# Kernel optimization log

Measured on AMD Instinct MI355X. Metric: run time of the kernel, lower is better.

The kernel has to match this reference:

```python
import jax, jax.numpy as jnp
import numpy as np

E, H, F, T, K = 32, 1024, 512, 1024, 8

def setup_inputs() -> dict:
    key = jax.random.key(0)
    k1, k2, k3, k4, k5 = jax.random.split(key, 5)
    return {
        "hidden_states": jax.random.normal(k1, (T, H), dtype=jnp.float32),
        "top_k_index": jax.random.randint(k2, (T, K), 0, E),
        "top_k_weights": jax.random.uniform(k3, (T, K), dtype=jnp.float32),
        "gate_up_proj": jax.random.normal(k4, (E, 2 * F, H), dtype=jnp.float32),
        "down_proj": jax.random.normal(k5, (E, H, F), dtype=jnp.float32),
    }

def reference(hidden_states, top_k_index, top_k_weights, gate_up_proj, down_proj):
    n_experts = gate_up_proj.shape[0]
    T_ = hidden_states.shape[0]
    # Combine routing weights into dense [T, E] map (duplicates accumulate,
    # matching torch's index_add_ semantics).
    w = jnp.zeros((T_, n_experts), dtype=hidden_states.dtype)
    w = w.at[jnp.arange(T_)[:, None], top_k_index].add(top_k_weights)
    ffn = down_proj.shape[-1]

    def step(final, params):
        Wgu, Wd, we = params  # [2F,H], [H,F], [T]
        gu = hidden_states @ Wgu.T            # [T, 2F]
        gate, up = gu[:, :ffn], gu[:, ffn:]
        out = (jax.nn.silu(gate) * up) @ Wd.T  # [T, H]
        return final + we[:, None] * out, None

    final, _ = jax.lax.scan(step, jnp.zeros_like(hidden_states),
                            (gate_up_proj, down_proj, w.T))
    return final
```

## Files before the change

kernel.cpp:

```cpp
#include <hip/hip_runtime.h>
#include <hip/hip_bf16.h>

#define NE     32
#define HD     1024
#define FF     512
#define NT     1024
#define TOPK   8
#define NPAIR  (NT * TOPK)
#define MAXT2  96

typedef __attribute__((ext_vector_type(8))) short  bf16x8;
typedef __attribute__((ext_vector_type(4))) float  f32x4;

__device__ __forceinline__ unsigned short f2bf_rne(float f) {
    unsigned u = __float_as_uint(f);
    u += 0x7FFFu + ((u >> 16) & 1u);
    return (unsigned short)(u >> 16);
}

__device__ __forceinline__ unsigned pk2(float x, float y) {
    __hip_bfloat162 h = __float22bfloat162_rn(float2{x, y});
    union { __hip_bfloat162 h; unsigned u; } c;
    c.h = h;
    return c.u;
}

__device__ __forceinline__ uint4 pk8(const float* __restrict__ p) {
    float4 a = *(const float4*)p;
    float4 b = *(const float4*)(p + 4);
    uint4 r;
    r.x = pk2(a.x, a.y);
    r.y = pk2(a.z, a.w);
    r.z = pk2(b.x, b.y);
    r.w = pk2(b.z, b.w);
    return r;
}


__global__ __launch_bounds__(1024) void k_route(const int* __restrict__ idx,
                                                const float* __restrict__ tkw,
                                                int* __restrict__ meta) {
    __shared__ int sc[NE], scur[NE], soff[NE + 1];
    __shared__ int ste[MAXT2], stm[MAXT2], snt;
    int tid = threadIdx.x;
    if (tid < NE) { sc[tid] = 0; scur[tid] = 0; }
    __syncthreads();
    int e8[TOPK];
#pragma unroll
    for (int j = 0; j < TOPK; j++) { e8[j] = idx[tid * TOPK + j]; atomicAdd(&sc[e8[j]], 1); }
    __syncthreads();
    if (tid == 0) {
        int off = 0, nt = 0;
        for (int e = 0; e < NE; e++) {
            soff[e] = off;
            for (int s = 0; s < sc[e]; s += 128) { ste[nt] = e; stm[nt] = s; nt++; }
            off += sc[e];
        }
        soff[NE] = off; snt = nt;
    }
    __syncthreads();
    int*   tok_list = meta + 256;
    float* w_list   = (float*)(meta + 8448);
    int*   posmap   = meta + 16640;
#pragma unroll
    for (int j = 0; j < TOPK; j++) {
        int e = e8[j];
        int p = soff[e] + atomicAdd(&scur[e], 1);
        tok_list[p] = tid;
        w_list[p]   = tkw[tid * TOPK + j];
        posmap[tid * TOPK + j] = p;
    }
    if (tid <= NE) meta[1 + tid] = soff[tid];
    if (tid == 0)  meta[0] = snt;
    if (tid < MAXT2) { meta[64 + tid] = (tid < snt) ? ste[tid] : 0;
                       meta[160 + tid] = (tid < snt) ? stm[tid] : 0; }
}

__global__ __launch_bounds__(256) void k_mm1(
        const float* __restrict__ hs, const float* __restrict__ wgu,
        const int* __restrict__ meta, unsigned short* __restrict__ A) {
    int numt = meta[0];
    int bx = blockIdx.x;
    if (bx >= numt) return;
    int e   = meta[64 + bx], m0 = meta[160 + bx];
    int seg = meta[1 + e];
    int nrows = meta[1 + e + 1] - seg - m0;
    if (nrows > 128) nrows = 128;
    int c0 = blockIdx.y * 64;
    const int* tok_list = meta + 256;
    const float* w_list = (const float*)(meta + 8448);

    __shared__ __align__(16) unsigned short Xs[128][40];
    __shared__ __align__(16) unsigned short Ws[128][40];
    __shared__ int   toks[128];
    __shared__ float wrow[128];
    int tid = threadIdx.x;
    if (tid < 128) {
        toks[tid] = (tid < nrows) ? tok_list[seg + m0 + tid] : -1;
        wrow[tid] = (tid < nrows) ? w_list[seg + m0 + tid] : 0.f;
    }
    __syncthreads();

    int wave = tid >> 6, lane = tid & 63, lr = lane & 15, lk = lane >> 4;
    f32x4 accg[2][4] = {}, accu[2][4] = {};
    const float* wbase = wgu + (size_t)e * 2 * FF * HD;

    for (int k0 = 0; k0 < HD; k0 += 32) {
        for (int c = tid; c < 512; c += 256) {
            int r = c >> 2, cc = c & 3;
            int tk = toks[r];
            uint4 xv = make_uint4(0, 0, 0, 0);
            if (tk >= 0) xv = pk8(hs + (size_t)tk * HD + k0 + cc * 8);
            *(uint4*)&Xs[r][cc * 8] = xv;
            int grow = (r < 64) ? (c0 + r) : (FF + c0 + (r - 64));
            *(uint4*)&Ws[r][cc * 8] = pk8(wbase + (size_t)grow * HD + k0 + cc * 8);
        }
        __syncthreads();
        bf16x8 a0 = *(const bf16x8*)&Xs[wave * 32 + lr][lk * 8];
        bf16x8 a1 = *(const bf16x8*)&Xs[wave * 32 + 16 + lr][lk * 8];
#pragma unroll
        for (int cf = 0; cf < 4; cf++) {
            bf16x8 bg = *(const bf16x8*)&Ws[cf * 16 + lr][lk * 8];
            bf16x8 bu = *(const bf16x8*)&Ws[64 + cf * 16 + lr][lk * 8];
            accg[0][cf] = __builtin_amdgcn_mfma_f32_16x16x32_bf16(a0, bg, accg[0][cf], 0, 0, 0);
            accg[1][cf] = __builtin_amdgcn_mfma_f32_16x16x32_bf16(a1, bg, accg[1][cf], 0, 0, 0);
            accu[0][cf] = __builtin_amdgcn_mfma_f32_16x16x32_bf16(a0, bu, accu[0][cf], 0, 0, 0);
            accu[1][cf] = __builtin_amdgcn_mfma_f32_16x16x32_bf16(a1, bu, accu[1][cf], 0, 0, 0);
        }
        __syncthreads();
    }
#pragma unroll
    for (int rf = 0; rf < 2; rf++)
#pragma unroll
        for (int q = 0; q < 4; q++) {
            int r = wave * 32 + rf * 16 + lk * 4 + q;
            if (r < nrows) {
                float w = wrow[r];
#pragma unroll
                for (int cf = 0; cf < 4; cf++) {
                    float g = accg[rf][cf][q], u = accu[rf][cf][q];
                    float act = (g / (1.f + __expf(-g))) * u * w;
                    A[(size_t)(seg + m0 + r) * FF + c0 + cf * 16 + lr] = f2bf_rne(act);
                }
            }
        }
}

__global__ __launch_bounds__(256) void k_mm2(
        const unsigned short* __restrict__ A, const float* __restrict__ wd,
        const int* __restrict__ meta, float* __restrict__ O) {
    int numt = meta[0];
    int bx = blockIdx.x;
    if (bx >= numt) return;
    int e   = meta[64 + bx], m0 = meta[160 + bx];
    int seg = meta[1 + e];
    int nrows = meta[1 + e + 1] - seg - m0;
    if (nrows > 128) nrows = 128;
    int n0 = blockIdx.y * 128;

    __shared__ __align__(16) unsigned short Xs[128][40];
    __shared__ __align__(16) unsigned short Ws[128][40];
    int tid = threadIdx.x;
    int wave = tid >> 6, lane = tid & 63, lr = lane & 15, lk = lane >> 4;
    f32x4 acc[2][8] = {};
    const float* wbase = wd + (size_t)e * HD * FF;

    for (int k0 = 0; k0 < FF; k0 += 32) {
        for (int c = tid; c < 512; c += 256) {
            int r = c >> 2, cc = c & 3;
            uint4 xv = make_uint4(0, 0, 0, 0);
            if (r < nrows) xv = *(const uint4*)(A + (size_t)(seg + m0 + r) * FF + k0 + cc * 8);
            *(uint4*)&Xs[r][cc * 8] = xv;
            *(uint4*)&Ws[r][cc * 8] = pk8(wbase + (size_t)(n0 + r) * FF + k0 + cc * 8);
        }
        __syncthreads();
        bf16x8 a0 = *(const bf16x8*)&Xs[wave * 32 + lr][lk * 8];
        bf16x8 a1 = *(const bf16x8*)&Xs[wave * 32 + 16 + lr][lk * 8];
#pragma unroll
        for (int cf = 0; cf < 8; cf++) {
            bf16x8 b = *(const bf16x8*)&Ws[cf * 16 + lr][lk * 8];
            acc[0][cf] = __builtin_amdgcn_mfma_f32_16x16x32_bf16(a0, b, acc[0][cf], 0, 0, 0);
            acc[1][cf] = __builtin_amdgcn_mfma_f32_16x16x32_bf16(a1, b, acc[1][cf], 0, 0, 0);
        }
        __syncthreads();
    }
#pragma unroll
    for (int rf = 0; rf < 2; rf++)
#pragma unroll
        for (int q = 0; q < 4; q++) {
            int r = wave * 32 + rf * 16 + lk * 4 + q;
            if (r < nrows) {
#pragma unroll
                for (int cf = 0; cf < 8; cf++)
                    O[(size_t)(seg + m0 + r) * HD + n0 + cf * 16 + lr] = acc[rf][cf][q];
            }
        }
}

__global__ void k_reduce(const float* __restrict__ O, const int* __restrict__ posmap,
                         float* __restrict__ out) {
    int i = blockIdx.x * blockDim.x + threadIdx.x;
    int t = i >> 8, c4 = i & 255;
    float4 acc = make_float4(0.f, 0.f, 0.f, 0.f);
#pragma unroll
    for (int k = 0; k < TOPK; k++) {
        int p = posmap[t * TOPK + k];
        float4 v = ((const float4*)(O + (size_t)p * HD))[c4];
        acc.x += v.x; acc.y += v.y; acc.z += v.z; acc.w += v.w;
    }
    ((float4*)out)[i] = acc;
}

extern "C" void kernel_launch(void* const* d_in, const int* in_sizes, int n_in,
                              void* d_out, int out_size, void* d_ws, size_t ws_size,
                              hipStream_t stream) {
    const float* hs  = (const float*)d_in[0];
    const int*   idx = (const int*)  d_in[1];
    const float* tkw = (const float*)d_in[2];
    const float* wgu = (const float*)d_in[3];
    const float* wd  = (const float*)d_in[4];
    float* out = (float*)d_out;

    const size_t OFF_A = 128 * 1024;
    const size_t OFF_O = OFF_A + (size_t)NPAIR * FF * 2;

    char* ws = (char*)d_ws;
    int* meta = (int*)ws;
    unsigned short* A_bf = (unsigned short*)(ws + OFF_A);
    float* O_rows        = (float*)(ws + OFF_O);
    const int* posmap    = meta + 16640;

    k_route<<<1, 1024, 0, stream>>>(idx, tkw, meta);
    dim3 g1(MAXT2, FF / 64);
    k_mm1<<<g1, 256, 0, stream>>>(hs, wgu, meta, A_bf);
    dim3 g2(MAXT2, HD / 128);
    k_mm2<<<g2, 256, 0, stream>>>(A_bf, wd, meta, O_rows);
    k_reduce<<<NT * HD / 4 / 256, 256, 0, stream>>>(O_rows, posmap, out);
}
```

Measured before the change: 133.6 us.

## Double-buffer LDS tiles, halve N-tile width, and swizzle block order in grouped GEMMs

Both grouped GEMM kernels now prefetch the next K-slice from global memory into registers while MFMAs run on the current LDS buffer. Each iteration writes into a second LDS buffer, so one barrier per iteration is removed. The output-column tile is halved, doubling the grid, and block indices are remapped so that neighbouring blocks share experts and rows for L2 reuse. The trade-off is that each weight tile's X rows are loaded twice as often, and each block does less MFMA work per iteration.

New measurement: 393.3 us. +194.4%, slower.

```diff
diff --git a/kernel.cpp b/kernel.cpp
--- a/kernel.cpp
+++ b/kernel.cpp
@@ -17,24 +17,19 @@
     u += 0x7FFFu + ((u >> 16) & 1u);
     return (unsigned short)(u >> 16);
 }
-
 __device__ __forceinline__ unsigned pk2(float x, float y) {
     __hip_bfloat162 h = __float22bfloat162_rn(float2{x, y});
     union { __hip_bfloat162 h; unsigned u; } c;
     c.h = h;
     return c.u;
 }
-
-__device__ __forceinline__ uint4 pk8(const float* __restrict__ p) {
-    float4 a = *(const float4*)p;
-    float4 b = *(const float4*)(p + 4);
+__device__ __forceinline__ uint4 pk8v(float4 a, float4 b) {
     uint4 r;
-    r.x = pk2(a.x, a.y);
-    r.y = pk2(a.z, a.w);
-    r.z = pk2(b.x, b.y);
-    r.w = pk2(b.z, b.w);
+    r.x = pk2(a.x, a.y); r.y = pk2(a.z, a.w);
+    r.z = pk2(b.x, b.y); r.w = pk2(b.z, b.w);
     return r;
 }
+#define MFMA16(a, b, c) __builtin_amdgcn_mfma_f32_16x16x32_bf16(a, b, c, 0, 0, 0)
 
 
 __global__ __launch_bounds__(1024) void k_route(const int* __restrict__ idx,
@@ -79,55 +74,86 @@
 __global__ __launch_bounds__(256) void k_mm1(
         const float* __restrict__ hs, const float* __restrict__ wgu,
         const int* __restrict__ meta, unsigned short* __restrict__ A) {
+    int lid = blockIdx.y * MAXT2 + blockIdx.x;
+    int wsw = (lid & 7) * 192 + (lid >> 3);
+    int bx = wsw % MAXT2, by = wsw / MAXT2;
     int numt = meta[0];
-    int bx = blockIdx.x;
     if (bx >= numt) return;
     int e   = meta[64 + bx], m0 = meta[160 + bx];
     int seg = meta[1 + e];
-    int nrows = meta[1 + e + 1] - seg - m0;
+    int nrows = meta[2 + e] - seg - m0;
     if (nrows > 128) nrows = 128;
-    int c0 = blockIdx.y * 64;
+    int c0 = by * 32;
+
+    __shared__ __align__(16) unsigned short Xs[2][128][40];
+    __shared__ __align__(16) unsigned short Ws[2][64][40];
+    __shared__ int   toks[128];
+    __shared__ float wrows[128];
+    int tid = threadIdx.x;
     const int* tok_list = meta + 256;
     const float* w_list = (const float*)(meta + 8448);
-
-    __shared__ __align__(16) unsigned short Xs[128][40];
-    __shared__ __align__(16) unsigned short Ws[128][40];
-    __shared__ int   toks[128];
-    __shared__ float wrow[128];
-    int tid = threadIdx.x;
     if (tid < 128) {
-        toks[tid] = (tid < nrows) ? tok_list[seg + m0 + tid] : -1;
-        wrow[tid] = (tid < nrows) ? w_list[seg + m0 + tid] : 0.f;
-    }
-    __syncthreads();
+        toks[tid]  = (tid < nrows) ? tok_list[seg + m0 + tid] : -1;
+        wrows[tid] = (tid < nrows) ? w_list[seg + m0 + tid] : 0.f;
+    }
+    __syncthreads();
+
+    int xr1 = tid >> 2, xc = (tid & 3) * 8;
+    int xr2 = xr1 + 64;
+    int tk1 = toks[xr1], tk2 = toks[xr2];
+    const float* xp1 = hs + (size_t)tk1 * HD + xc;
+    const float* xp2 = hs + (size_t)tk2 * HD + xc;
+    int wr = tid >> 2;
+    int wg_row = (wr < 32) ? (c0 + wr) : (FF + c0 + (wr - 32));
+    const float* wp = wgu + (size_t)e * (2 * FF) * HD + (size_t)wg_row * HD + xc;
 
     int wave = tid >> 6, lane = tid & 63, lr = lane & 15, lk = lane >> 4;
-    f32x4 accg[2][4] = {}, accu[2][4] = {};
-    const float* wbase = wgu + (size_t)e * 2 * FF * HD;
-
+    f32x4 accg[2][2] = {}, accu[2][2] = {};
+    const float4 z4 = {0.f, 0.f, 0.f, 0.f};
+
+    {
+        float4 a1 = tk1 >= 0 ? *(const float4*)(xp1)     : z4;
+        float4 b1 = tk1 >= 0 ? *(const float4*)(xp1 + 4) : z4;
+        float4 a2 = tk2 >= 0 ? *(const float4*)(xp2)     : z4;
+        float4 b2 = tk2 >= 0 ? *(const float4*)(xp2 + 4) : z4;
+        float4 wa = *(const float4*)(wp), wb = *(const float4*)(wp + 4);
+        *(uint4*)&Xs[0][xr1][xc] = pk8v(a1, b1);
+        *(uint4*)&Xs[0][xr2][xc] = pk8v(a2, b2);
+        *(uint4*)&Ws[0][wr][xc]  = pk8v(wa, wb);
+    }
+    __syncthreads();
+
+    int cur = 0;
     for (int k0 = 0; k0 < HD; k0 += 32) {
-        for (int c = tid; c < 512; c += 256) {
-            int r = c >> 2, cc = c & 3;
-            int tk = toks[r];
-            uint4 xv = make_uint4(0, 0, 0, 0);
-            if (tk >= 0) xv = pk8(hs + (size_t)tk * HD + k0 + cc * 8);
-            *(uint4*)&Xs[r][cc * 8] = xv;
-            int grow = (r < 64) ? (c0 + r) : (FF + c0 + (r - 64));
-            *(uint4*)&Ws[r][cc * 8] = pk8(wbase + (size_t)grow * HD + k0 + cc * 8);
+        bool more = (k0 + 32) < HD;
+        float4 a1, b1, a2, b2, wa, wb;
+        if (more) {
+            int k = k0 + 32;
+            a1 = tk1 >= 0 ? *(const float4*)(xp1 + k)     : z4;
+            b1 = tk1 >= 0 ? *(const float4*)(xp1 + k + 4) : z4;
+            a2 = tk2 >= 0 ? *(const float4*)(xp2 + k)     : z4;
+            b2 = tk2 >= 0 ? *(const float4*)(xp2 + k + 4) : z4;
+            wa = *(const float4*)(wp + k);
+            wb = *(const float4*)(wp + k + 4);
+        }
+        bf16x8 fa0 = *(const bf16x8*)&Xs[cur][wave * 32 + lr][lk * 8];
+        bf16x8 fa1 = *(const bf16x8*)&Xs[cur][wave * 32 + 16 + lr][lk * 8];
+#pragma unroll
+        for (int cf = 0; cf < 2; cf++) {
+            bf16x8 bg = *(const bf16x8*)&Ws[cur][cf * 16 + lr][lk * 8];
+            bf16x8 bu = *(const bf16x8*)&Ws[cur][32 + cf * 16 + lr][lk * 8];
+            accg[0][cf] = MFMA16(fa0, bg, accg[0][cf]);
+            accg[1][cf] = MFMA16(fa1, bg, accg[1][cf]);
+            accu[0][cf] = MFMA16(fa0, bu, accu[0][cf]);
+            accu[1][cf] = MFMA16(fa1, bu, accu[1][cf]);
+        }
+        if (more) {
+            *(uint4*)&Xs[cur ^ 1][xr1][xc] = pk8v(a1, b1);
+            *(uint4*)&Xs[cur ^ 1][xr2][xc] = pk8v(a2, b2);
+            *(uint4*)&Ws[cur ^ 1][wr][xc]  = pk8v(wa, wb);
         }
         __syncthreads();
-        bf16x8 a0 = *(const bf16x8*)&Xs[wave * 32 + lr][lk * 8];
-        bf16x8 a1 = *(const bf16x8*)&Xs[wave * 32 + 16 + lr][lk * 8];
-#pragma unroll
-        for (int cf = 0; cf < 4; cf++) {
-            bf16x8 bg = *(const bf16x8*)&Ws[cf * 16 + lr][lk * 8];
-            bf16x8 bu = *(const bf16x8*)&Ws[64 + cf * 16 + lr][lk * 8];
-            accg[0][cf] = __builtin_amdgcn_mfma_f32_16x16x32_bf16(a0, bg, accg[0][cf], 0, 0, 0);
-            accg[1][cf] = __builtin_amdgcn_mfma_f32_16x16x32_bf16(a1, bg, accg[1][cf], 0, 0, 0);
-            accu[0][cf] = __builtin_amdgcn_mfma_f32_16x16x32_bf16(a0, bu, accu[0][cf], 0, 0, 0);
-            accu[1][cf] = __builtin_amdgcn_mfma_f32_16x16x32_bf16(a1, bu, accu[1][cf], 0, 0, 0);
-        }
-        __syncthreads();
+        cur ^= 1;
     }
 #pragma unroll
     for (int rf = 0; rf < 2; rf++)
@@ -135,9 +161,9 @@
         for (int q = 0; q < 4; q++) {
             int r = wave * 32 + rf * 16 + lk * 4 + q;
             if (r < nrows) {
-                float w = wrow[r];
-#pragma unroll
-                for (int cf = 0; cf < 4; cf++) {
+                float w = wrows[r];
+#pragma unroll
+                for (int cf = 0; cf < 2; cf++) {
                     float g = accg[rf][cf][q], u = accu[rf][cf][q];
                     float act = (g / (1.f + __expf(-g))) * u * w;
                     A[(size_t)(seg + m0 + r) * FF + c0 + cf * 16 + lr] = f2bf_rne(act);
@@ -149,40 +175,68 @@
 __global__ __launch_bounds__(256) void k_mm2(
         const unsigned short* __restrict__ A, const float* __restrict__ wd,
         const int* __restrict__ meta, float* __restrict__ O) {
+    int lid = blockIdx.y * MAXT2 + blockIdx.x;
+    int wsw = (lid & 7) * 192 + (lid >> 3);
+    int bx = wsw % MAXT2, by = wsw / MAXT2;
     int numt = meta[0];
-    int bx = blockIdx.x;
     if (bx >= numt) return;
     int e   = meta[64 + bx], m0 = meta[160 + bx];
     int seg = meta[1 + e];
-    int nrows = meta[1 + e + 1] - seg - m0;
+    int nrows = meta[2 + e] - seg - m0;
     if (nrows > 128) nrows = 128;
-    int n0 = blockIdx.y * 128;
-
-    __shared__ __align__(16) unsigned short Xs[128][40];
-    __shared__ __align__(16) unsigned short Ws[128][40];
+    int n0 = by * 64;
+
+    __shared__ __align__(16) unsigned short Xs[2][128][40];
+    __shared__ __align__(16) unsigned short Ws[2][64][40];
     int tid = threadIdx.x;
+    int xr1 = tid >> 2, xc = (tid & 3) * 8;
+    int xr2 = xr1 + 64;
+    bool v1 = xr1 < nrows, v2 = xr2 < nrows;
+    const unsigned short* ap1 = A + (size_t)(seg + m0 + xr1) * FF + xc;
+    const unsigned short* ap2 = A + (size_t)(seg + m0 + xr2) * FF + xc;
+    int wr = tid >> 2;
+    const float* wp = wd + (size_t)e * HD * FF + (size_t)(n0 + wr) * FF + xc;
+
     int wave = tid >> 6, lane = tid & 63, lr = lane & 15, lk = lane >> 4;
-    f32x4 acc[2][8] = {};
-    const float* wbase = wd + (size_t)e * HD * FF;
-
+    f32x4 acc[2][4] = {};
+    const uint4  zu = {0u, 0u, 0u, 0u};
+
+    {
+        uint4 x1 = v1 ? *(const uint4*)(ap1) : zu;
+        uint4 x2 = v2 ? *(const uint4*)(ap2) : zu;
+        float4 wa = *(const float4*)(wp), wb = *(const float4*)(wp + 4);
+        *(uint4*)&Xs[0][xr1][xc] = x1;
+        *(uint4*)&Xs[0][xr2][xc] = x2;
+        *(uint4*)&Ws[0][wr][xc]  = pk8v(wa, wb);
+    }
+    __syncthreads();
+
+    int cur = 0;
     for (int k0 = 0; k0 < FF; k0 += 32) {
-        for (int c = tid; c < 512; c += 256) {
-            int r = c >> 2, cc = c & 3;
-            uint4 xv = make_uint4(0, 0, 0, 0);
-            if (r < nrows) xv = *(const uint4*)(A + (size_t)(seg + m0 + r) * FF + k0 + cc * 8);
-            *(uint4*)&Xs[r][cc * 8] = xv;
-            *(uint4*)&Ws[r][cc * 8] = pk8(wbase + (size_t)(n0 + r) * FF + k0 + cc * 8);
+        bool more = (k0 + 32) < FF;
+        uint4 x1, x2; float4 wa, wb;
+        if (more) {
+            int k = k0 + 32;
+            x1 = v1 ? *(const uint4*)(ap1 + k) : zu;
+            x2 = v2 ? *(const uint4*)(ap2 + k) : zu;
+            wa = *(const float4*)(wp + k);
+            wb = *(const float4*)(wp + k + 4);
+        }
+        bf16x8 fa0 = *(const bf16x8*)&Xs[cur][wave * 32 + lr][lk * 8];
+        bf16x8 fa1 = *(const bf16x8*)&Xs[cur][wave * 32 + 16 + lr][lk * 8];
+#pragma unroll
+        for (int cf = 0; cf < 4; cf++) {
+            bf16x8 b = *(const bf16x8*)&Ws[cur][cf * 16 + lr][lk * 8];
+            acc[0][cf] = MFMA16(fa0, b, acc[0][cf]);
+            acc[1][cf] = MFMA16(fa1, b, acc[1][cf]);
+        }
+        if (more) {
+            *(uint4*)&Xs[cur ^ 1][xr1][xc] = x1;
+            *(uint4*)&Xs[cur ^ 1][xr2][xc] = x2;
+            *(uint4*)&Ws[cur ^ 1][wr][xc]  = pk8v(wa, wb);
         }
         __syncthreads();
-        bf16x8 a0 = *(const bf16x8*)&Xs[wave * 32 + lr][lk * 8];
-        bf16x8 a1 = *(const bf16x8*)&Xs[wave * 32 + 16 + lr][lk * 8];
-#pragma unroll
-        for (int cf = 0; cf < 8; cf++) {
-            bf16x8 b = *(const bf16x8*)&Ws[cf * 16 + lr][lk * 8];
-            acc[0][cf] = __builtin_amdgcn_mfma_f32_16x16x32_bf16(a0, b, acc[0][cf], 0, 0, 0);
-            acc[1][cf] = __builtin_amdgcn_mfma_f32_16x16x32_bf16(a1, b, acc[1][cf], 0, 0, 0);
-        }
-        __syncthreads();
+        cur ^= 1;
     }
 #pragma unroll
     for (int rf = 0; rf < 2; rf++)
@@ -191,7 +245,7 @@
             int r = wave * 32 + rf * 16 + lk * 4 + q;
             if (r < nrows) {
 #pragma unroll
-                for (int cf = 0; cf < 8; cf++)
+                for (int cf = 0; cf < 4; cf++)
                     O[(size_t)(seg + m0 + r) * HD + n0 + cf * 16 + lr] = acc[rf][cf][q];
             }
         }
@@ -231,9 +285,9 @@
     const int* posmap    = meta + 16640;
 
     k_route<<<1, 1024, 0, stream>>>(idx, tkw, meta);
-    dim3 g1(MAXT2, FF / 64);
+    dim3 g1(MAXT2, FF / 32);
     k_mm1<<<g1, 256, 0, stream>>>(hs, wgu, meta, A_bf);
-    dim3 g2(MAXT2, HD / 128);
+    dim3 g2(MAXT2, HD / 64);
     k_mm2<<<g2, 256, 0, stream>>>(A_bf, wd, meta, O_rows);
     k_reduce<<<NT * HD / 4 / 256, 256, 0, stream>>>(O_rows, posmap, out);
 }
```

## Pre-gather bf16 tokens and pipeline MoE GEMMs with direct-to-LDS triple buffering

Applied to the files above, without the earlier changes.

Adds a gather kernel that converts routed token rows to bf16 once. Both grouped GEMMs now stream activations with global_load_lds into a triple-buffered, XOR-swizzled LDS ring, and keep weights in registers with a double-buffered prefetch, so there is one barrier per k-step instead of two. Block indices are remapped so blocks sharing an expert run close together, and the kernels use launch bounds for two blocks per CU. The aim is to hide global latency and stop converting the same fp32 activations repeatedly per column tile. In exchange it adds a kernel launch and an extra bf16 workspace, and relies on hand-written vmcnt waits being correct.

Result: slower. 140.6 us (+5.3%).

```diff
diff --git a/kernel.cpp b/kernel.cpp
--- a/kernel.cpp
+++ b/kernel.cpp
@@ -17,25 +17,40 @@
     u += 0x7FFFu + ((u >> 16) & 1u);
     return (unsigned short)(u >> 16);
 }
-
 __device__ __forceinline__ unsigned pk2(float x, float y) {
     __hip_bfloat162 h = __float22bfloat162_rn(float2{x, y});
     union { __hip_bfloat162 h; unsigned u; } c;
     c.h = h;
     return c.u;
 }
-
-__device__ __forceinline__ uint4 pk8(const float* __restrict__ p) {
-    float4 a = *(const float4*)p;
-    float4 b = *(const float4*)(p + 4);
+__device__ __forceinline__ uint4 pk8q(float4 a, float4 b) {
     uint4 r;
-    r.x = pk2(a.x, a.y);
-    r.y = pk2(a.z, a.w);
-    r.z = pk2(b.x, b.y);
-    r.w = pk2(b.z, b.w);
+    r.x = pk2(a.x, a.y); r.y = pk2(a.z, a.w);
+    r.z = pk2(b.x, b.y); r.w = pk2(b.z, b.w);
     return r;
 }
-
+__device__ __forceinline__ bf16x8 pk8r(float4 a, float4 b) {
+    union { unsigned u[4]; bf16x8 v; } r;
+    r.u[0] = pk2(a.x, a.y); r.u[1] = pk2(a.z, a.w);
+    r.u[2] = pk2(b.x, b.y); r.u[3] = pk2(b.z, b.w);
+    return r.v;
+}
+__device__ __forceinline__ void gload16(const void* g, void* l) {
+    __builtin_amdgcn_global_load_lds(
+        (const __attribute__((address_space(1))) unsigned int*)g,
+        (__attribute__((address_space(3))) unsigned int*)l, 16, 0, 0);
+}
+#define MFMA16(a, b, c) __builtin_amdgcn_mfma_f32_16x16x32_bf16(a, b, c, 0, 0, 0)
+
+#define PIPE_SYNC() do {                                   \
+    asm volatile("s_waitcnt vmcnt(6)" ::: "memory");       \
+    __builtin_amdgcn_s_barrier();                          \
+    __builtin_amdgcn_sched_barrier(0);                     \
+} while (0)
+
+#define OFF_XG (128u * 1024u)
+#define OFF_AB (OFF_XG + 8320u * 2048u)
+#define OFF_O  (OFF_AB + 8320u * 1024u)
 
 __global__ __launch_bounds__(1024) void k_route(const int* __restrict__ idx,
                                                 const float* __restrict__ tkw,
@@ -76,123 +91,210 @@
                        meta[160 + tid] = (tid < snt) ? stm[tid] : 0; }
 }
 
-__global__ __launch_bounds__(256) void k_mm1(
-        const float* __restrict__ hs, const float* __restrict__ wgu,
-        const int* __restrict__ meta, unsigned short* __restrict__ A) {
+__global__ void k_gather(const float* __restrict__ hs, const int* __restrict__ meta,
+                         unsigned short* __restrict__ Xg) {
+    int i = blockIdx.x * blockDim.x + threadIdx.x;
+    int p = i >> 7, c = (i & 127) << 3;
+    int tok = meta[256 + p];
+    float4 a = *(const float4*)(hs + (size_t)tok * HD + c);
+    float4 b = *(const float4*)(hs + (size_t)tok * HD + c + 4);
+    *(uint4*)(Xg + (size_t)p * HD + c) = pk8q(a, b);
+}
+
+__global__ __launch_bounds__(256, 2) void k_mm1(
+        const unsigned short* __restrict__ Xg, const float* __restrict__ wgu,
+        const int* __restrict__ meta, const float* __restrict__ w_list,
+        unsigned short* __restrict__ A) {
+    int lid = blockIdx.x;
+    int wsw = (lid & 7) * 96 + (lid >> 3);
+    int bx = wsw >> 3, by = wsw & 7;
     int numt = meta[0];
-    int bx = blockIdx.x;
     if (bx >= numt) return;
     int e   = meta[64 + bx], m0 = meta[160 + bx];
     int seg = meta[1 + e];
-    int nrows = meta[1 + e + 1] - seg - m0;
+    int nrows = meta[2 + e] - seg - m0;
     if (nrows > 128) nrows = 128;
-    int c0 = blockIdx.y * 64;
-    const int* tok_list = meta + 256;
-    const float* w_list = (const float*)(meta + 8448);
-
-    __shared__ __align__(16) unsigned short Xs[128][40];
-    __shared__ __align__(16) unsigned short Ws[128][40];
-    __shared__ int   toks[128];
-    __shared__ float wrow[128];
+    int c0 = by * 64;
+
+    __shared__ __align__(16) unsigned char Xb0[8192];
+    __shared__ __align__(16) unsigned char Xb1[8192];
+    __shared__ __align__(16) unsigned char Xb2[8192];
     int tid = threadIdx.x;
-    if (tid < 128) {
-        toks[tid] = (tid < nrows) ? tok_list[seg + m0 + tid] : -1;
-        wrow[tid] = (tid < nrows) ? w_list[seg + m0 + tid] : 0.f;
-    }
-    __syncthreads();
-
     int wave = tid >> 6, lane = tid & 63, lr = lane & 15, lk = lane >> 4;
-    f32x4 accg[2][4] = {}, accu[2][4] = {};
-    const float* wbase = wgu + (size_t)e * 2 * FF * HD;
-
-    for (int k0 = 0; k0 < HD; k0 += 32) {
-        for (int c = tid; c < 512; c += 256) {
-            int r = c >> 2, cc = c & 3;
-            int tk = toks[r];
-            uint4 xv = make_uint4(0, 0, 0, 0);
-            if (tk >= 0) xv = pk8(hs + (size_t)tk * HD + k0 + cc * 8);
-            *(uint4*)&Xs[r][cc * 8] = xv;
-            int grow = (r < 64) ? (c0 + r) : (FF + c0 + (r - 64));
-            *(uint4*)&Ws[r][cc * 8] = pk8(wbase + (size_t)grow * HD + k0 + cc * 8);
-        }
-        __syncthreads();
-        bf16x8 a0 = *(const bf16x8*)&Xs[wave * 32 + lr][lk * 8];
-        bf16x8 a1 = *(const bf16x8*)&Xs[wave * 32 + 16 + lr][lk * 8];
-#pragma unroll
-        for (int cf = 0; cf < 4; cf++) {
-            bf16x8 bg = *(const bf16x8*)&Ws[cf * 16 + lr][lk * 8];
-            bf16x8 bu = *(const bf16x8*)&Ws[64 + cf * 16 + lr][lk * 8];
-            accg[0][cf] = __builtin_amdgcn_mfma_f32_16x16x32_bf16(a0, bg, accg[0][cf], 0, 0, 0);
-            accg[1][cf] = __builtin_amdgcn_mfma_f32_16x16x32_bf16(a1, bg, accg[1][cf], 0, 0, 0);
-            accu[0][cf] = __builtin_amdgcn_mfma_f32_16x16x32_bf16(a0, bu, accu[0][cf], 0, 0, 0);
-            accu[1][cf] = __builtin_amdgcn_mfma_f32_16x16x32_bf16(a1, bu, accu[1][cf], 0, 0, 0);
-        }
-        __syncthreads();
-    }
-#pragma unroll
-    for (int rf = 0; rf < 2; rf++)
+
+    unsigned Lp0 = (unsigned)(wave * 2) * 1024u + (unsigned)lane * 16u;
+    unsigned Lp1 = Lp0 + 1024u;
+    unsigned ldsoff0 = Lp0, ldsoff1 = Lp1;
+    const unsigned char* xsrc0 = (const unsigned char*)Xg +
+        (size_t)(seg + m0 + (Lp0 >> 6)) * (HD * 2) + ((Lp0 & 63u) ^ (((Lp0 >> 7) & 3u) << 4));
+    const unsigned char* xsrc1 = (const unsigned char*)Xg +
+        (size_t)(seg + m0 + (Lp1 >> 6)) * (HD * 2) + ((Lp1 & 63u) ^ (((Lp1 >> 7) & 3u) << 4));
+
+    int cp = c0 + wave * 16 + lr;
+    const float* gp = wgu + ((size_t)e * 2 * FF + cp) * HD + lk * 8;
+    const float* up = gp + (size_t)FF * HD;
+
+    unsigned aoff[8];
+#pragma unroll
+    for (int mf = 0; mf < 8; mf++) {
+        unsigned row = mf * 16 + lr;
+        aoff[mf] = row * 64 + (((unsigned)lk * 16) ^ (((row >> 1) & 3u) << 4));
+    }
+
+    f32x4 acc[8][2] = {};
+    float4 wsA[4], wsB[4];
+    const unsigned char* cur = Xb0;
+    const unsigned char* nxt = Xb1;
+    const unsigned char* fut = Xb2;
+
+    gload16(xsrc0, Xb0 + ldsoff0); gload16(xsrc1, Xb0 + ldsoff1);
+    xsrc0 += 64; xsrc1 += 64;
+    gload16(xsrc0, Xb1 + ldsoff0); gload16(xsrc1, Xb1 + ldsoff1);
+    xsrc0 += 64; xsrc1 += 64;
+    wsA[0] = *(const float4*)(gp);     wsA[1] = *(const float4*)(gp + 4);
+    wsA[2] = *(const float4*)(up);     wsA[3] = *(const float4*)(up + 4);
+    int wk = 32;
+
+    auto step = [&](float4 (&wuse)[4], float4 (&wld)[4], bool doX, bool doW) {
+        PIPE_SYNC();
+        if (doX) {
+            gload16(xsrc0, (void*)(fut + ldsoff0));
+            gload16(xsrc1, (void*)(fut + ldsoff1));
+            xsrc0 += 64; xsrc1 += 64;
+        }
+        if (doW) {
+            wld[0] = *(const float4*)(gp + wk);     wld[1] = *(const float4*)(gp + wk + 4);
+            wld[2] = *(const float4*)(up + wk);     wld[3] = *(const float4*)(up + wk + 4);
+            wk += 32;
+        }
+        bf16x8 bg = pk8r(wuse[0], wuse[1]);
+        bf16x8 bu = pk8r(wuse[2], wuse[3]);
+#pragma unroll
+        for (int mf = 0; mf < 8; mf++) {
+            bf16x8 af = *(const bf16x8*)(cur + aoff[mf]);
+            acc[mf][0] = MFMA16(af, bg, acc[mf][0]);
+            acc[mf][1] = MFMA16(af, bu, acc[mf][1]);
+        }
+        const unsigned char* t = cur; cur = nxt; nxt = fut; fut = t;
+    };
+
+    for (int t2 = 0; t2 < 14; t2++) {
+        step(wsA, wsB, true, true);
+        step(wsB, wsA, true, true);
+    }
+    step(wsA, wsB, true,  true);
+    step(wsB, wsA, true,  true);
+    step(wsA, wsB, false, true);
+    step(wsB, wsA, false, false);
+
+#pragma unroll
+    for (int mf = 0; mf < 8; mf++)
 #pragma unroll
         for (int q = 0; q < 4; q++) {
-            int r = wave * 32 + rf * 16 + lk * 4 + q;
+            int r = mf * 16 + lk * 4 + q;
             if (r < nrows) {
-                float w = wrow[r];
-#pragma unroll
-                for (int cf = 0; cf < 4; cf++) {
-                    float g = accg[rf][cf][q], u = accu[rf][cf][q];
-                    float act = (g / (1.f + __expf(-g))) * u * w;
-                    A[(size_t)(seg + m0 + r) * FF + c0 + cf * 16 + lr] = f2bf_rne(act);
-                }
+                float w = w_list[seg + m0 + r];
+                float g = acc[mf][0][q], u = acc[mf][1][q];
+                float act = (g / (1.f + __expf(-g))) * u * w;
+                A[(size_t)(seg + m0 + r) * FF + cp] = f2bf_rne(act);
             }
         }
 }
 
-__global__ __launch_bounds__(256) void k_mm2(
+__global__ __launch_bounds__(256, 2) void k_mm2(
         const unsigned short* __restrict__ A, const float* __restrict__ wd,
         const int* __restrict__ meta, float* __restrict__ O) {
+    int lid = blockIdx.x;
+    int wsw = (lid & 7) * 96 + (lid >> 3);
+    int bx = wsw >> 3, by = wsw & 7;
     int numt = meta[0];
-    int bx = blockIdx.x;
     if (bx >= numt) return;
     int e   = meta[64 + bx], m0 = meta[160 + bx];
     int seg = meta[1 + e];
-    int nrows = meta[1 + e + 1] - seg - m0;
+    int nrows = meta[2 + e] - seg - m0;
     if (nrows > 128) nrows = 128;
-    int n0 = blockIdx.y * 128;
-
-    __shared__ __align__(16) unsigned short Xs[128][40];
-    __shared__ __align__(16) unsigned short Ws[128][40];
+    int n0 = by * 128;
+
+    __shared__ __align__(16) unsigned char Xb0[8192];
+    __shared__ __align__(16) unsigned char Xb1[8192];
+    __shared__ __align__(16) unsigned char Xb2[8192];
     int tid = threadIdx.x;
     int wave = tid >> 6, lane = tid & 63, lr = lane & 15, lk = lane >> 4;
-    f32x4 acc[2][8] = {};
-    const float* wbase = wd + (size_t)e * HD * FF;
-
-    for (int k0 = 0; k0 < FF; k0 += 32) {
-        for (int c = tid; c < 512; c += 256) {
-            int r = c >> 2, cc = c & 3;
-            uint4 xv = make_uint4(0, 0, 0, 0);
-            if (r < nrows) xv = *(const uint4*)(A + (size_t)(seg + m0 + r) * FF + k0 + cc * 8);
-            *(uint4*)&Xs[r][cc * 8] = xv;
-            *(uint4*)&Ws[r][cc * 8] = pk8(wbase + (size_t)(n0 + r) * FF + k0 + cc * 8);
-        }
-        __syncthreads();
-        bf16x8 a0 = *(const bf16x8*)&Xs[wave * 32 + lr][lk * 8];
-        bf16x8 a1 = *(const bf16x8*)&Xs[wave * 32 + 16 + lr][lk * 8];
-#pragma unroll
-        for (int cf = 0; cf < 8; cf++) {
-            bf16x8 b = *(const bf16x8*)&Ws[cf * 16 + lr][lk * 8];
-            acc[0][cf] = __builtin_amdgcn_mfma_f32_16x16x32_bf16(a0, b, acc[0][cf], 0, 0, 0);
-            acc[1][cf] = __builtin_amdgcn_mfma_f32_16x16x32_bf16(a1, b, acc[1][cf], 0, 0, 0);
-        }
-        __syncthreads();
-    }
-#pragma unroll
-    for (int rf = 0; rf < 2; rf++)
+
+    unsigned Lp0 = (unsigned)(wave * 2) * 1024u + (unsigned)lane * 16u;
+    unsigned Lp1 = Lp0 + 1024u;
+    unsigned ldsoff0 = Lp0, ldsoff1 = Lp1;
+    const unsigned char* xsrc0 = (const unsigned char*)A +
+        (size_t)(seg + m0 + (Lp0 >> 6)) * (FF * 2) + ((Lp0 & 63u) ^ (((Lp0 >> 7) & 3u) << 4));
+    const unsigned char* xsrc1 = (const unsigned char*)A +
+        (size_t)(seg + m0 + (Lp1 >> 6)) * (FF * 2) + ((Lp1 & 63u) ^ (((Lp1 >> 7) & 3u) << 4));
+
+    int n_a = n0 + wave * 32 + lr;
+    int n_b = n_a + 16;
+    const float* wpa = wd + ((size_t)e * HD + n_a) * FF + lk * 8;
+    const float* wpb = wd + ((size_t)e * HD + n_b) * FF + lk * 8;
+
+    unsigned aoff[8];
+#pragma unroll
+    for (int mf = 0; mf < 8; mf++) {
+        unsigned row = mf * 16 + lr;
+        aoff[mf] = row * 64 + (((unsigned)lk * 16) ^ (((row >> 1) & 3u) << 4));
+    }
+
+    f32x4 acc[8][2] = {};
+    float4 wsA[4], wsB[4];
+    const unsigned char* cur = Xb0;
+    const unsigned char* nxt = Xb1;
+    const unsigned char* fut = Xb2;
+
+    gload16(xsrc0, Xb0 + ldsoff0); gload16(xsrc1, Xb0 + ldsoff1);
+    xsrc0 += 64; xsrc1 += 64;
+    gload16(xsrc0, Xb1 + ldsoff0); gload16(xsrc1, Xb1 + ldsoff1);
+    xsrc0 += 64; xsrc1 += 64;
+    wsA[0] = *(const float4*)(wpa);    wsA[1] = *(const float4*)(wpa + 4);
+    wsA[2] = *(const float4*)(wpb);    wsA[3] = *(const float4*)(wpb + 4);
+    int wk = 32;
+
+    auto step = [&](float4 (&wuse)[4], float4 (&wld)[4], bool doX, bool doW) {
+        PIPE_SYNC();
+        if (doX) {
+            gload16(xsrc0, (void*)(fut + ldsoff0));
+            gload16(xsrc1, (void*)(fut + ldsoff1));
+            xsrc0 += 64; xsrc1 += 64;
+        }
+        if (doW) {
+            wld[0] = *(const float4*)(wpa + wk);   wld[1] = *(const float4*)(wpa + wk + 4);
+            wld[2] = *(const float4*)(wpb + wk);   wld[3] = *(const float4*)(wpb + wk + 4);
+            wk += 32;
+        }
+        bf16x8 b0 = pk8r(wuse[0], wuse[1]);
+        bf16x8 b1 = pk8r(wuse[2], wuse[3]);
+#pragma unroll
+        for (int mf = 0; mf < 8; mf++) {
+            bf16x8 af = *(const bf16x8*)(cur + aoff[mf]);
+            acc[mf][0] = MFMA16(af, b0, acc[mf][0]);
+            acc[mf][1] = MFMA16(af, b1, acc[mf][1]);
+        }
+        const unsigned char* t = cur; cur = nxt; nxt = fut; fut = t;
+    };
+
+    for (int t2 = 0; t2 < 6; t2++) {
+        step(wsA, wsB, true, true);
+        step(wsB, wsA, true, true);
+    }
+    step(wsA, wsB, true,  true);
+    step(wsB, wsA, true,  true);
+    step(wsA, wsB, false, true);
+    step(wsB, wsA, false, false);
+
+#pragma unroll
+    for (int mf = 0; mf < 8; mf++)
 #pragma unroll
         for (int q = 0; q < 4; q++) {
-            int r = wave * 32 + rf * 16 + lk * 4 + q;
+            int r = mf * 16 + lk * 4 + q;
             if (r < nrows) {
-#pragma unroll
-                for (int cf = 0; cf < 8; cf++)
-                    O[(size_t)(seg + m0 + r) * HD + n0 + cf * 16 + lr] = acc[rf][cf][q];
+                O[(size_t)(seg + m0 + r) * HD + n_a] = acc[mf][0][q];
+                O[(size_t)(seg + m0 + r) * HD + n_b] = acc[mf][1][q];
             }
         }
 }
@@ -221,19 +323,17 @@
     const float* wd  = (const float*)d_in[4];
     float* out = (float*)d_out;
 
-    const size_t OFF_A = 128 * 1024;
-    const size_t OFF_O = OFF_A + (size_t)NPAIR * FF * 2;
-
     char* ws = (char*)d_ws;
     int* meta = (int*)ws;
-    unsigned short* A_bf = (unsigned short*)(ws + OFF_A);
+    unsigned short* Xg   = (unsigned short*)(ws + OFF_XG);
+    unsigned short* A_bf = (unsigned short*)(ws + OFF_AB);
     float* O_rows        = (float*)(ws + OFF_O);
+    const float* w_list  = (const float*)(meta + 8448);
     const int* posmap    = meta + 16640;
 
     k_route<<<1, 1024, 0, stream>>>(idx, tkw, meta);
-    dim3 g1(MAXT2, FF / 64);
-    k_mm1<<<g1, 256, 0, stream>>>(hs, wgu, meta, A_bf);
-    dim3 g2(MAXT2, HD / 128);
-    k_mm2<<<g2, 256, 0, stream>>>(A_bf, wd, meta, O_rows);
+    k_gather<<<NPAIR * (HD / 8) / 256, 256, 0, stream>>>(hs, meta, Xg);
+    k_mm1<<<MAXT2 * 8, 256, 0, stream>>>(Xg, wgu, meta, w_list, A_bf);
+    k_mm2<<<MAXT2 * 8, 256, 0, stream>>>(A_bf, wd, meta, O_rows);
     k_reduce<<<NT * HD / 4 / 256, 256, 0, stream>>>(O_rows, posmap, out);
 }
```
